# Performance work log

Hardware: AMD Instinct MI355X
Metric: run time of the kernel (lower is better)

Reference implementation:

```python
import jax, jax.numpy as jnp
import numpy as np

B, C, H, W = 4, 64, 64, 64

def setup_inputs() -> dict:
    key = jax.random.key(0)
    ks = jax.random.split(key, 9)
    return {
        "x": jax.random.normal(ks[0], (B, C, H, W), dtype=jnp.float32),
        "Wq": jax.random.normal(ks[1], (C, C), dtype=jnp.float32) * (1.0 / np.sqrt(C)),
        "bq": jax.random.normal(ks[2], (C,), dtype=jnp.float32) * 0.02,
        "Wk": jax.random.normal(ks[3], (C, C), dtype=jnp.float32) * (1.0 / np.sqrt(C)),
        "bk": jax.random.normal(ks[4], (C,), dtype=jnp.float32) * 0.02,
        "Wv": jax.random.normal(ks[5], (C, C), dtype=jnp.float32) * (1.0 / np.sqrt(C)),
        "bv": jax.random.normal(ks[6], (C,), dtype=jnp.float32) * 0.02,
        "rel_h": jax.random.normal(ks[7], (1, C, H, 1), dtype=jnp.float32),
        "rel_w": jax.random.normal(ks[8], (1, C, 1, W), dtype=jnp.float32),
    }

def reference(x, Wq, bq, Wk, bk, Wv, bv, rel_h, rel_w):
    b, c, h, w = x.shape
    n = h * w
    xf = x.reshape(b, c, n)                                  # [B,C,N]
    # 1x1 convs == channel-wise linear maps (weight [out,in])
    q = jnp.einsum('oc,bcn->bno', Wq, xf) + bq               # [B,N,C]
    k = jnp.einsum('oc,bcn->bon', Wk, xf) + bk[:, None]      # [B,C,N]
    v = jnp.einsum('oc,bcn->bon', Wv, xf) + bv[:, None]      # [B,C,N]
    energy = jnp.einsum('bnc,bcm->bnm', q, k)                # content term [B,N,N]
    pos = (rel_h + rel_w).reshape(c, n)                      # [C,N]
    energy = energy + jnp.einsum('bnc,cm->bnm', q, pos)      # add positional bias
    attn = jax.nn.softmax(energy, axis=-1)                   # [B,N,N]
    # out[b,c,n] = sum_m v[b,c,m] * attn[b,n,m]  (bmm with attention^T)
    out = jnp.einsum('bcm,bnm->bcn', v, attn)
    return out.reshape(b, c, h, w)
```

## Files before the change

### kernel.cpp

```cpp
#include <hip/hip_runtime.h>
#include <math.h>

#define NPOS 4096
#define NB   4
#define NROW (NB * NPOS)
#define LOG2E 1.44269504088896f

typedef _Float16 f16;
typedef f16 f16x4 __attribute__((ext_vector_type(4)));
typedef f16 f16x8 __attribute__((ext_vector_type(8)));
typedef float f32x4 __attribute__((ext_vector_type(4)));
typedef float f32x16 __attribute__((ext_vector_type(16)));

#define LDW 72

__global__ __launch_bounds__(256) void qkv_proj(
    const float* __restrict__ x,
    const float* __restrict__ Wq, const float* __restrict__ bq,
    const float* __restrict__ Wk, const float* __restrict__ bk,
    const float* __restrict__ Wv, const float* __restrict__ bv,
    const float* __restrict__ rel_h, const float* __restrict__ rel_w,
    f16* __restrict__ qh, f16* __restrict__ kh, f16* __restrict__ vh)
{
    __shared__ __align__(16) f16 Ws[192 * LDW];
    __shared__ __align__(16) f16 Xs[32 * LDW];
    __shared__ __align__(16) f16 Vs[64 * 36];

    const int tid = threadIdx.x;
    const int b   = blockIdx.x >> 7;
    const int n0  = (blockIdx.x & 127) << 5;

    #pragma unroll
    for (int k = 0; k < 12; ++k) {
        int idx  = tid + k * 256;
        int orow = idx >> 4;
        int cseg = (idx & 15) << 2;
        int mat  = orow >> 6;
        int o    = orow & 63;
        const float* wsrc = (mat == 0) ? Wq : ((mat == 1) ? Wk : Wv);
        float4 v = *(const float4*)(wsrc + o * 64 + cseg);
        f16x4 h; h[0] = (f16)v.x; h[1] = (f16)v.y; h[2] = (f16)v.z; h[3] = (f16)v.w;
        *(f16x4*)(&Ws[orow * LDW + cseg]) = h;
    }
    {
        int c  = tid >> 2;
        int ns = (tid & 3) << 3;
        const float* xp = x + ((size_t)(b * 64 + c)) * NPOS + n0 + ns;
        float4 v0 = *(const float4*)(xp);
        float4 v1 = *(const float4*)(xp + 4);
        Xs[(ns + 0) * LDW + c] = (f16)v0.x;
        Xs[(ns + 1) * LDW + c] = (f16)v0.y;
        Xs[(ns + 2) * LDW + c] = (f16)v0.z;
        Xs[(ns + 3) * LDW + c] = (f16)v0.w;
        Xs[(ns + 4) * LDW + c] = (f16)v1.x;
        Xs[(ns + 5) * LDW + c] = (f16)v1.y;
        Xs[(ns + 6) * LDW + c] = (f16)v1.z;
        Xs[(ns + 7) * LDW + c] = (f16)v1.w;
    }
    __syncthreads();

    const int wave = tid >> 6;
    const int lane = tid & 63;
    const int quad = lane >> 4;
    const int l16  = lane & 15;
    const int rg   = wave >> 1;
    const int tb   = (wave & 1) * 6;

    const f16x8 a0 = *(const f16x8*)(&Xs[(rg * 16 + l16) * LDW + quad * 8]);
    const f16x8 a1 = *(const f16x8*)(&Xs[(rg * 16 + l16) * LDW + 32 + quad * 8]);

    f32x4 acc[6];
    #pragma unroll
    for (int i = 0; i < 6; ++i) {
        int t = tb + i;
        f32x4 c0 = {0, 0, 0, 0};
        f16x8 b0 = *(const f16x8*)(&Ws[(t * 16 + l16) * LDW + quad * 8]);
        f16x8 b1 = *(const f16x8*)(&Ws[(t * 16 + l16) * LDW + 32 + quad * 8]);
        c0 = __builtin_amdgcn_mfma_f32_16x16x32_f16(a0, b0, c0, 0, 0, 0);
        c0 = __builtin_amdgcn_mfma_f32_16x16x32_f16(a1, b1, c0, 0, 0, 0);
        acc[i] = c0;
    }

    #pragma unroll
    for (int i = 0; i < 6; ++i) {
        int t = tb + i;
        if (t < 4) {
            int o = t * 16 + l16;
            float bb = bq[o];
            #pragma unroll
            for (int r = 0; r < 4; ++r) {
                size_t n = (size_t)b * NPOS + n0 + rg * 16 + quad * 4 + r;
                qh[n * 64 + o] = (f16)((acc[i][r] + bb) * LOG2E);
            }
        } else if (t < 8) {
            int o = (t - 4) * 16 + l16;
            int h = n0 >> 6;
            int wbase = (n0 & 63) + rg * 16;
            float bb = bk[o] + rel_h[o * 64 + h];
            #pragma unroll
            for (int r = 0; r < 4; ++r) {
                size_t n = (size_t)b * NPOS + n0 + rg * 16 + quad * 4 + r;
                kh[n * 64 + o] = (f16)(acc[i][r] + bb + rel_w[o * 64 + wbase + quad * 4 + r]);
            }
        } else {
            int o = (t - 8) * 16 + l16;
            float bb = bv[o];
            #pragma unroll
            for (int r = 0; r < 4; ++r)
                Vs[o * 36 + rg * 16 + quad * 4 + r] = (f16)(acc[i][r] + bb);
        }
    }
    __syncthreads();
    {
        int c  = tid >> 2;
        int ns = (tid & 3) << 3;
        f16x8 vv = *(const f16x8*)(&Vs[c * 36 + ns]);
        *(f16x8*)(vh + ((size_t)(b * 64 + c)) * NPOS + n0 + ns) = vv;
    }
}

__global__ __launch_bounds__(256, 4) void attn(
    const f16* __restrict__ qh, const f16* __restrict__ kh,
    const f16* __restrict__ vh,
    f16* __restrict__ Op, float* __restrict__ Mp, float* __restrict__ Lp,
    int split, int mchunk)
{
    __shared__ __align__(16) f16 Ks[2][64 * 64];
    __shared__ __align__(16) f16 Vt[2][64 * 64];

    const int tid  = threadIdx.x;
    const int wv   = tid >> 6;
    const int lane = tid & 63;
    const int l31  = lane & 31;
    const int hi   = lane >> 5;
    const int sw   = l31 & 7;
    const int s    = blockIdx.x % split;
    const int tile = blockIdx.x / split;
    const int b    = tile >> 5;
    const int n0   = (tile & 31) << 7;
    const int n_lane = n0 + wv * 32 + l31;

    f16x8 bq[4];
    {
        const f16* qbase = qh + ((size_t)b * NPOS + n_lane) * 64 + hi * 8;
        #pragma unroll
        for (int kc = 0; kc < 4; ++kc) bq[kc] = *(const f16x8*)(qbase + kc * 16);
    }

    f32x16 O0 = {}, O1 = {};
    float m_i = -1e30f, l_i = 0.f;

    const f16* kb = kh + (size_t)b * NPOS * 64;
    const f16* vb = vh + (size_t)b * 64 * NPOS;

    const int m_begin = s * mchunk;
    for (int m0 = m_begin; m0 < m_begin + mchunk; m0 += 128) {
        #pragma unroll
        for (int h = 0; h < 2; ++h) {
            #pragma unroll
            for (int q = 0; q < 2; ++q) {
                const int idx  = q * 256 + tid;
                const int row  = idx >> 3;
                const int slot = (idx & 7) ^ (row & 7);
                __builtin_amdgcn_global_load_lds(
                    (const __attribute__((address_space(1))) void*)
                        (kb + (size_t)(m0 + h * 64 + row) * 64 + slot * 8),
                    (__attribute__((address_space(3))) void*)
                        (&Ks[h][(q * 4 + wv) * 512]),
                    16, 0, 0);
                __builtin_amdgcn_global_load_lds(
                    (const __attribute__((address_space(1))) void*)
                        (vb + (size_t)row * NPOS + m0 + h * 64 + slot * 8),
                    (__attribute__((address_space(3))) void*)
                        (&Vt[h][(q * 4 + wv) * 512]),
                    16, 0, 0);
            }
        }
        __syncthreads();

        #pragma unroll
        for (int h = 0; h < 2; ++h) {
            f32x16 S0 = {}, S1 = {};
            #pragma unroll
            for (int kc = 0; kc < 4; ++kc) {
                const int so = ((kc * 2 + hi) ^ sw) << 3;
                f16x8 ak0 = *(const f16x8*)(&Ks[h][l31 * 64 + so]);
                f16x8 ak1 = *(const f16x8*)(&Ks[h][(32 + l31) * 64 + so]);
                S0 = __builtin_amdgcn_mfma_f32_32x32x16_f16(ak0, bq[kc], S0, 0, 0, 0);
                S1 = __builtin_amdgcn_mfma_f32_32x32x16_f16(ak1, bq[kc], S1, 0, 0, 0);
            }

            float tm[8];
            #pragma unroll
            for (int r = 0; r < 8; ++r)
                tm[r] = fmaxf(fmaxf(S0[r], S0[r + 8]), fmaxf(S1[r], S1[r + 8]));
            #pragma unroll
            for (int st = 4; st > 0; st >>= 1)
                #pragma unroll
                for (int r = 0; r < st; ++r) tm[r] = fmaxf(tm[r], tm[r + st]);
            float mx = fmaxf(tm[0], __shfl_xor(tm[0], 32));

            if (__any(mx > m_i)) {
                const float mn = fmaxf(m_i, mx);
                const float al = __builtin_amdgcn_exp2f(m_i - mn);
                m_i = mn;
                l_i *= al;
                #pragma unroll
                for (int r = 0; r < 16; ++r) { O0[r] *= al; O1[r] *= al; }
            }

            float rs = 0.f;
            #pragma unroll
            for (int mc = 0; mc < 4; ++mc) {
                f16x8 pb;
                #pragma unroll
                for (int j = 0; j < 8; ++j) {
                    const float sv = (mc < 2) ? S0[(mc & 1) * 8 + j]
                                              : S1[(mc & 1) * 8 + j];
                    const float e = __builtin_amdgcn_exp2f(sv - m_i);
                    rs += e;
                    pb[j] = (f16)e;
                }
                const int s0off = (((mc * 2)     ^ sw) << 3) + (hi << 2);
                const int s1off = (((mc * 2 + 1) ^ sw) << 3) + (hi << 2);
                {
                    const f16* vrow = &Vt[h][l31 * 64];
                    union { f16x8 v8; f16x4 v4[2]; } av;
                    av.v4[0] = *(const f16x4*)(vrow + s0off);
                    av.v4[1] = *(const f16x4*)(vrow + s1off);
                    O0 = __builtin_amdgcn_mfma_f32_32x32x16_f16(av.v8, pb, O0, 0, 0, 0);
                }
                {
                    const f16* vrow = &Vt[h][(32 + l31) * 64];
                    union { f16x8 v8; f16x4 v4[2]; } av;
                    av.v4[0] = *(const f16x4*)(vrow + s0off);
                    av.v4[1] = *(const f16x4*)(vrow + s1off);
                    O1 = __builtin_amdgcn_mfma_f32_32x32x16_f16(av.v8, pb, O1, 0, 0, 0);
                }
            }
            rs += __shfl_xor(rs, 32);
            l_i += rs;
        }
        __syncthreads();
    }

    const float inv = 1.f / l_i;
    f16* opb = Op + (((size_t)s * NB + b) * 64) * NPOS + n_lane;
    #pragma unroll
    for (int r = 0; r < 16; ++r) {
        const int c0 = (r & 3) + ((r >> 2) << 3) + (hi << 2);
        opb[(size_t)c0 * NPOS]        = (f16)(O0[r] * inv);
        opb[(size_t)(c0 + 32) * NPOS] = (f16)(O1[r] * inv);
    }
    if (hi == 0) {
        const size_t row = (size_t)b * NPOS + n_lane;
        Mp[(size_t)s * NROW + row] = m_i;
        Lp[(size_t)s * NROW + row] = l_i;
    }
}

__global__ __launch_bounds__(256) void combine(
    const f16* __restrict__ Op, const float* __restrict__ Mp,
    const float* __restrict__ Lp, float* __restrict__ out, int split)
{
    __shared__ float Wn[8][32];

    const int tid = threadIdx.x;
    const int b   = blockIdx.x >> 7;
    const int n0  = (blockIdx.x & 127) << 5;

    if (tid < 32) {
        const size_t row = (size_t)b * NPOS + n0 + tid;
        float M = -1e30f;
        for (int s2 = 0; s2 < split; ++s2)
            M = fmaxf(M, Mp[(size_t)s2 * NROW + row]);
        float L = 0.f;
        for (int s2 = 0; s2 < split; ++s2) {
            const float w = Lp[(size_t)s2 * NROW + row] *
                            __builtin_amdgcn_exp2f(Mp[(size_t)s2 * NROW + row] - M);
            Wn[s2][tid] = w;
            L += w;
        }
        const float inv = 1.f / L;
        for (int s2 = 0; s2 < split; ++s2) Wn[s2][tid] *= inv;
    }
    __syncthreads();

    const int c  = tid >> 2;
    const int ns = (tid & 3) << 3;
    float acc[8] = {0.f, 0.f, 0.f, 0.f, 0.f, 0.f, 0.f, 0.f};
    for (int s2 = 0; s2 < split; ++s2) {
        const f16x8 a = *(const f16x8*)(Op + (((size_t)s2 * NB + b) * 64 + c) * NPOS + n0 + ns);
        #pragma unroll
        for (int j = 0; j < 8; ++j) acc[j] += Wn[s2][ns + j] * (float)a[j];
    }
    float* po = out + ((size_t)(b * 64 + c)) * NPOS + n0 + ns;
    float4 o0 = {acc[0], acc[1], acc[2], acc[3]};
    float4 o1 = {acc[4], acc[5], acc[6], acc[7]};
    *(float4*)(po)     = o0;
    *(float4*)(po + 4) = o1;
}

extern "C" void kernel_launch(void* const* d_in, const int* in_sizes, int n_in,
                              void* d_out, int out_size, void* d_ws, size_t ws_size,
                              hipStream_t stream) {
    const float* x     = (const float*)d_in[0];
    const float* Wq    = (const float*)d_in[1];
    const float* bq    = (const float*)d_in[2];
    const float* Wk    = (const float*)d_in[3];
    const float* bk    = (const float*)d_in[4];
    const float* Wv    = (const float*)d_in[5];
    const float* bv    = (const float*)d_in[6];
    const float* rel_h = (const float*)d_in[7];
    const float* rel_w = (const float*)d_in[8];
    float* out = (float*)d_out;

    const size_t qkv_elems = (size_t)NROW * 64;
    int split = 8;
    {
        size_t need = 3 * qkv_elems * sizeof(f16)
                    + (size_t)split * NROW * 64 * sizeof(f16)
                    + 2 * (size_t)split * NROW * sizeof(float);
        if (ws_size < need) split = 4;
    }
    const int mchunk = NPOS / split;

    f16* qh = (f16*)d_ws;
    f16* kh = qh + qkv_elems;
    f16* vh = kh + qkv_elems;
    f16* Op = vh + qkv_elems;
    float* Mp = (float*)(Op + (size_t)split * NROW * 64);
    float* Lp = Mp + (size_t)split * NROW;

    qkv_proj<<<NB * (NPOS / 32), 256, 0, stream>>>(x, Wq, bq, Wk, bk, Wv, bv,
                                                   rel_h, rel_w, qh, kh, vh);
    attn<<<NB * (NPOS / 128) * split, 256, 0, stream>>>(qh, kh, vh, Op, Mp, Lp,
                                                        split, mchunk);
    combine<<<NB * (NPOS / 32), 256, 0, stream>>>(Op, Mp, Lp, out, split);
}
```

Measured before the change: 115.0 us.

## Double-buffer K/V tiles in attention and coalesce Q/K projection stores

The attention loop changes from loading a 128-key block and then computing on it to a 64-key double-buffered pipeline, where the next tile is prefetched with global_load_lds while the current one is computed. This is meant to hide global-to-LDS latency behind MFMA and softmax work. The online-softmax rescale now runs only when the running max grows by more than 8 (log2 units), which skips most rescales. The projection kernel stages Q and K through reused LDS and writes them as 16-byte vectors instead of scattered 2-byte stores. Costs are one barrier per 64 keys instead of per 128, and the lazy rescale lets exponent values reach up to 2^8, which could affect fp16 precision of P.

```diff
diff --git a/kernel.cpp b/kernel.cpp
--- a/kernel.cpp
+++ b/kernel.cpp
@@ -13,6 +13,7 @@
 typedef float f32x16 __attribute__((ext_vector_type(16)));
 
 #define LDW 72
+#define LDQ 68
 
 __global__ __launch_bounds__(256) void qkv_proj(
     const float* __restrict__ x,
@@ -24,7 +25,6 @@
 {
     __shared__ __align__(16) f16 Ws[192 * LDW];
     __shared__ __align__(16) f16 Xs[32 * LDW];
-    __shared__ __align__(16) f16 Vs[64 * 36];
 
     const int tid = threadIdx.x;
     const int b   = blockIdx.x >> 7;
@@ -80,6 +80,11 @@
         c0 = __builtin_amdgcn_mfma_f32_16x16x32_f16(a1, b1, c0, 0, 0, 0);
         acc[i] = c0;
     }
+    __syncthreads();
+
+    f16* Qs  = Ws;
+    f16* Kst = Ws + 32 * LDQ;
+    f16* Vs  = Ws + 64 * LDQ;
 
     #pragma unroll
     for (int i = 0; i < 6; ++i) {
@@ -88,20 +93,17 @@
             int o = t * 16 + l16;
             float bb = bq[o];
             #pragma unroll
-            for (int r = 0; r < 4; ++r) {
-                size_t n = (size_t)b * NPOS + n0 + rg * 16 + quad * 4 + r;
-                qh[n * 64 + o] = (f16)((acc[i][r] + bb) * LOG2E);
-            }
+            for (int r = 0; r < 4; ++r)
+                Qs[(rg * 16 + quad * 4 + r) * LDQ + o] = (f16)((acc[i][r] + bb) * LOG2E);
         } else if (t < 8) {
             int o = (t - 4) * 16 + l16;
-            int h = n0 >> 6;
+            int hh = n0 >> 6;
             int wbase = (n0 & 63) + rg * 16;
-            float bb = bk[o] + rel_h[o * 64 + h];
-            #pragma unroll
-            for (int r = 0; r < 4; ++r) {
-                size_t n = (size_t)b * NPOS + n0 + rg * 16 + quad * 4 + r;
-                kh[n * 64 + o] = (f16)(acc[i][r] + bb + rel_w[o * 64 + wbase + quad * 4 + r]);
-            }
+            float bb = bk[o] + rel_h[o * 64 + hh];
+            #pragma unroll
+            for (int r = 0; r < 4; ++r)
+                Kst[(rg * 16 + quad * 4 + r) * LDQ + o] =
+                    (f16)(acc[i][r] + bb + rel_w[o * 64 + wbase + quad * 4 + r]);
         } else {
             int o = (t - 8) * 16 + l16;
             float bb = bv[o];
@@ -111,6 +113,13 @@
         }
     }
     __syncthreads();
+    {
+        int nl = tid >> 3;
+        int cs = (tid & 7) << 3;
+        size_t gro = ((size_t)b * NPOS + n0 + nl) * 64 + cs;
+        *(f16x8*)(qh + gro) = *(const f16x8*)(&Qs[nl * LDQ + cs]);
+        *(f16x8*)(kh + gro) = *(const f16x8*)(&Kst[nl * LDQ + cs]);
+    }
     {
         int c  = tid >> 2;
         int ns = (tid & 3) << 3;
@@ -154,94 +163,100 @@
     const f16* vb = vh + (size_t)b * 64 * NPOS;
 
     const int m_begin = s * mchunk;
-    for (int m0 = m_begin; m0 < m_begin + mchunk; m0 += 128) {
-        #pragma unroll
-        for (int h = 0; h < 2; ++h) {
-            #pragma unroll
-            for (int q = 0; q < 2; ++q) {
-                const int idx  = q * 256 + tid;
-                const int row  = idx >> 3;
-                const int slot = (idx & 7) ^ (row & 7);
-                __builtin_amdgcn_global_load_lds(
-                    (const __attribute__((address_space(1))) void*)
-                        (kb + (size_t)(m0 + h * 64 + row) * 64 + slot * 8),
-                    (__attribute__((address_space(3))) void*)
-                        (&Ks[h][(q * 4 + wv) * 512]),
-                    16, 0, 0);
-                __builtin_amdgcn_global_load_lds(
-                    (const __attribute__((address_space(1))) void*)
-                        (vb + (size_t)row * NPOS + m0 + h * 64 + slot * 8),
-                    (__attribute__((address_space(3))) void*)
-                        (&Vt[h][(q * 4 + wv) * 512]),
-                    16, 0, 0);
+    const int T = mchunk >> 6;
+
+    auto STAGE = [&](int t, int pb) {
+        const int m0 = m_begin + (t << 6);
+        #pragma unroll
+        for (int q = 0; q < 2; ++q) {
+            const int idx  = q * 256 + tid;
+            const int row  = idx >> 3;
+            const int slot = (idx & 7) ^ (row & 7);
+            __builtin_amdgcn_global_load_lds(
+                (const __attribute__((address_space(1))) void*)
+                    (kb + (size_t)(m0 + row) * 64 + slot * 8),
+                (__attribute__((address_space(3))) void*)
+                    (&Ks[pb][(q * 4 + wv) * 512]),
+                16, 0, 0);
+            __builtin_amdgcn_global_load_lds(
+                (const __attribute__((address_space(1))) void*)
+                    (vb + (size_t)row * NPOS + m0 + slot * 8),
+                (__attribute__((address_space(3))) void*)
+                    (&Vt[pb][(q * 4 + wv) * 512]),
+                16, 0, 0);
+        }
+    };
+
+    int cur = 0;
+    STAGE(0, 0);
+    __syncthreads();
+
+    for (int t = 0; t < T; ++t) {
+        if (t + 1 < T) STAGE(t + 1, cur ^ 1);
+
+        f32x16 S0 = {}, S1 = {};
+        #pragma unroll
+        for (int kc = 0; kc < 4; ++kc) {
+            const int so = ((kc * 2 + hi) ^ sw) << 3;
+            f16x8 ak0 = *(const f16x8*)(&Ks[cur][l31 * 64 + so]);
+            f16x8 ak1 = *(const f16x8*)(&Ks[cur][(32 + l31) * 64 + so]);
+            S0 = __builtin_amdgcn_mfma_f32_32x32x16_f16(ak0, bq[kc], S0, 0, 0, 0);
+            S1 = __builtin_amdgcn_mfma_f32_32x32x16_f16(ak1, bq[kc], S1, 0, 0, 0);
+        }
+
+        float tm[8];
+        #pragma unroll
+        for (int r = 0; r < 8; ++r)
+            tm[r] = fmaxf(fmaxf(S0[r], S0[r + 8]), fmaxf(S1[r], S1[r + 8]));
+        #pragma unroll
+        for (int st = 4; st > 0; st >>= 1)
+            #pragma unroll
+            for (int r = 0; r < st; ++r) tm[r] = fmaxf(tm[r], tm[r + st]);
+        float mx = fmaxf(tm[0], __shfl_xor(tm[0], 32));
+
+        if (__any(mx > m_i + 8.f)) {
+            const float mn = fmaxf(m_i, mx);
+            const float al = __builtin_amdgcn_exp2f(m_i - mn);
+            m_i = mn;
+            l_i *= al;
+            #pragma unroll
+            for (int r = 0; r < 16; ++r) { O0[r] *= al; O1[r] *= al; }
+        }
+
+        float rs = 0.f;
+        #pragma unroll
+        for (int mc = 0; mc < 4; ++mc) {
+            f16x8 pb;
+            #pragma unroll
+            for (int j = 0; j < 8; ++j) {
+                const float sv = (mc < 2) ? S0[(mc & 1) * 8 + j]
+                                          : S1[(mc & 1) * 8 + j];
+                const float e = __builtin_amdgcn_exp2f(sv - m_i);
+                rs += e;
+                pb[j] = (f16)e;
             }
-        }
+            const int s0off = (((mc * 2)     ^ sw) << 3) + (hi << 2);
+            const int s1off = (((mc * 2 + 1) ^ sw) << 3) + (hi << 2);
+            {
+                const f16* vrow = &Vt[cur][l31 * 64];
+                union { f16x8 v8; f16x4 v4[2]; } av;
+                av.v4[0] = *(const f16x4*)(vrow + s0off);
+                av.v4[1] = *(const f16x4*)(vrow + s1off);
+                O0 = __builtin_amdgcn_mfma_f32_32x32x16_f16(av.v8, pb, O0, 0, 0, 0);
+            }
+            {
+                const f16* vrow = &Vt[cur][(32 + l31) * 64];
+                union { f16x8 v8; f16x4 v4[2]; } av;
+                av.v4[0] = *(const f16x4*)(vrow + s0off);
+                av.v4[1] = *(const f16x4*)(vrow + s1off);
+                O1 = __builtin_amdgcn_mfma_f32_32x32x16_f16(av.v8, pb, O1, 0, 0, 0);
+            }
+        }
+        rs += __shfl_xor(rs, 32);
+        l_i += rs;
+
         __syncthreads();
-
-        #pragma unroll
-        for (int h = 0; h < 2; ++h) {
-            f32x16 S0 = {}, S1 = {};
-            #pragma unroll
-            for (int kc = 0; kc < 4; ++kc) {
-                const int so = ((kc * 2 + hi) ^ sw) << 3;
-                f16x8 ak0 = *(const f16x8*)(&Ks[h][l31 * 64 + so]);
-                f16x8 ak1 = *(const f16x8*)(&Ks[h][(32 + l31) * 64 + so]);
-                S0 = __builtin_amdgcn_mfma_f32_32x32x16_f16(ak0, bq[kc], S0, 0, 0, 0);
-                S1 = __builtin_amdgcn_mfma_f32_32x32x16_f16(ak1, bq[kc], S1, 0, 0, 0);
-            }
-
-            float tm[8];
-            #pragma unroll
-            for (int r = 0; r < 8; ++r)
-                tm[r] = fmaxf(fmaxf(S0[r], S0[r + 8]), fmaxf(S1[r], S1[r + 8]));
-            #pragma unroll
-            for (int st = 4; st > 0; st >>= 1)
-                #pragma unroll
-                for (int r = 0; r < st; ++r) tm[r] = fmaxf(tm[r], tm[r + st]);
-            float mx = fmaxf(tm[0], __shfl_xor(tm[0], 32));
-
-            if (__any(mx > m_i)) {
-                const float mn = fmaxf(m_i, mx);
-                const float al = __builtin_amdgcn_exp2f(m_i - mn);
-                m_i = mn;
-                l_i *= al;
-                #pragma unroll
-                for (int r = 0; r < 16; ++r) { O0[r] *= al; O1[r] *= al; }
-            }
-
-            float rs = 0.f;
-            #pragma unroll
-            for (int mc = 0; mc < 4; ++mc) {
-                f16x8 pb;
-                #pragma unroll
-                for (int j = 0; j < 8; ++j) {
-                    const float sv = (mc < 2) ? S0[(mc & 1) * 8 + j]
-                                              : S1[(mc & 1) * 8 + j];
-                    const float e = __builtin_amdgcn_exp2f(sv - m_i);
-                    rs += e;
-                    pb[j] = (f16)e;
-                }
-                const int s0off = (((mc * 2)     ^ sw) << 3) + (hi << 2);
-                const int s1off = (((mc * 2 + 1) ^ sw) << 3) + (hi << 2);
-                {
-                    const f16* vrow = &Vt[h][l31 * 64];
-                    union { f16x8 v8; f16x4 v4[2]; } av;
-                    av.v4[0] = *(const f16x4*)(vrow + s0off);
-                    av.v4[1] = *(const f16x4*)(vrow + s1off);
-                    O0 = __builtin_amdgcn_mfma_f32_32x32x16_f16(av.v8, pb, O0, 0, 0, 0);
-                }
-                {
-                    const f16* vrow = &Vt[h][(32 + l31) * 64];
-                    union { f16x8 v8; f16x4 v4[2]; } av;
-                    av.v4[0] = *(const f16x4*)(vrow + s0off);
-                    av.v4[1] = *(const f16x4*)(vrow + s1off);
-                    O1 = __builtin_amdgcn_mfma_f32_32x32x16_f16(av.v8, pb, O1, 0, 0, 0);
-                }
-            }
-            rs += __shfl_xor(rs, 32);
-            l_i += rs;
-        }
-        __syncthreads();
+        cur ^= 1;
     }
 
     const float inv = 1.f / l_i;
```

Measured after the change: 115.1 us. Within noise of the previous version (+0.1%).
